# Optimization experiments

Hardware: AMD Instinct MI355X
Metric: run time of the kernel (lower is better)

Reference implementation:

```python
import jax, jax.numpy as jnp
import numpy as np

B, T, ENC, DEC, OUT = 512, 128, 256, 256, 1
Tm1 = T - 1


def setup_inputs() -> dict:
    key = jax.random.key(0)
    ks = jax.random.split(key, 14)
    s = lambda k, shape, scale=0.05: (jax.random.normal(k, shape, dtype=jnp.float32) * scale)
    return {
        "input_encoded": jax.random.normal(ks[0], (B, Tm1, ENC), dtype=jnp.float32),
        "y_history": jax.random.normal(ks[1], (B, Tm1, OUT), dtype=jnp.float32),
        # attn_layer: Linear(2*DEC+ENC -> ENC), Tanh, Linear(ENC -> 1)
        "W_attn1": s(ks[2], (ENC, 2 * DEC + ENC)),
        "b_attn1": s(ks[3], (ENC,)),
        "W_attn2": s(ks[4], (1, ENC)),
        "b_attn2": s(ks[5], (1,)),
        # single-layer LSTM cell (input_size=OUT, hidden=DEC); gate order i,f,g,o
        "W_ih": s(ks[6], (4 * DEC, OUT)),
        "W_hh": s(ks[7], (4 * DEC, DEC)),
        "b_ih": s(ks[8], (4 * DEC,)),
        "b_hh": s(ks[9], (4 * DEC,)),
        # fc: Linear(ENC+OUT -> OUT); torch code re-inits weight ~ N(0,1)
        "W_fc": jax.random.normal(ks[10], (OUT, ENC + OUT), dtype=jnp.float32),
        "b_fc": s(ks[11], (OUT,)),
        # fc_final: Linear(DEC+ENC -> OUT)
        "W_fcf": s(ks[12], (OUT, DEC + ENC)),
        "b_fcf": s(ks[13], (OUT,)),
    }


def reference(input_encoded, y_history, W_attn1, b_attn1, W_attn2, b_attn2,
              W_ih, W_hh, b_ih, b_hh, W_fc, b_fc, W_fcf, b_fcf):
    Bsz, tm1, enc = input_encoded.shape
    dec = W_hh.shape[1]
    h0 = jnp.zeros((Bsz, dec), dtype=input_encoded.dtype)
    c0 = jnp.zeros_like(h0)
    ctx0 = jnp.zeros((Bsz, enc), dtype=input_encoded.dtype)

    def step(carry, y_t):
        h, c, _ = carry  # h, c: [B, DEC]; y_t: [B, OUT]
        hs = jnp.broadcast_to(h[:, None, :], (Bsz, tm1, dec))
        cs = jnp.broadcast_to(c[:, None, :], (Bsz, tm1, dec))
        x = jnp.concatenate([hs, cs, input_encoded], axis=-1)  # [B, Tm1, 2*DEC+ENC]
        score = jnp.tanh(x @ W_attn1.T + b_attn1) @ W_attn2.T + b_attn2  # [B, Tm1, 1]
        attn = jax.nn.softmax(score[..., 0], axis=1)  # [B, Tm1]
        context = jnp.einsum('bt,bte->be', attn, input_encoded)  # [B, ENC]
        y_tilde = jnp.concatenate([context, y_t], axis=1) @ W_fc.T + b_fc  # [B, OUT]
        gates = y_tilde @ W_ih.T + b_ih + h @ W_hh.T + b_hh  # [B, 4*DEC]
        i, f, g, o = jnp.split(gates, 4, axis=1)
        c_new = jax.nn.sigmoid(f) * c + jax.nn.sigmoid(i) * jnp.tanh(g)
        h_new = jax.nn.sigmoid(o) * jnp.tanh(c_new)
        return (h_new, c_new, context), attn

    (h, c, context), attn_rows = jax.lax.scan(
        step, (h0, c0, ctx0), jnp.swapaxes(y_history, 0, 1))
    weight = jnp.swapaxes(attn_rows, 0, 1)  # [B, Tm1, Tm1]
    out = jnp.concatenate([h, context], axis=1) @ W_fcf.T + b_fcf  # [B, OUT]
    return out, weight
```

## Files before the change

kernel.cpp:

```cpp
#include <hip/hip_runtime.h>

typedef _Float16 f16;
typedef _Float16 h2 __attribute__((ext_vector_type(2)));
typedef _Float16 h4 __attribute__((ext_vector_type(4)));
typedef _Float16 h8 __attribute__((ext_vector_type(8)));

#define T127 127

#define H2S(v, i) __builtin_shufflevector(v, v, 2 * (i), 2 * (i) + 1)

__device__ __forceinline__ float rcp_f(float x) { return __builtin_amdgcn_rcpf(x); }

__device__ __forceinline__ float fdot2(h2 a, h2 b, float c) {
  return __builtin_amdgcn_fdot2(a, b, c, false);
}
__device__ __forceinline__ h2 mk2(f16 a, f16 b) { h2 v; v[0] = a; v[1] = b; return v; }

__device__ __forceinline__ float fast_sig(float x) {
  x = fminf(fmaxf(x, -30.f), 30.f);
  return rcp_f(1.f + __expf(-x));
}
__device__ __forceinline__ float fast_tanh(float x) {
  x = fminf(fmaxf(x, -12.f), 12.f);
  float e = __expf(2.f * x);
  return (e - 1.f) * rcp_f(e + 1.f);
}

__device__ __forceinline__ void bar_lds() {
  asm volatile("s_waitcnt lgkmcnt(0)" ::: "memory");
  __builtin_amdgcn_s_barrier();
  asm volatile("" ::: "memory");
}

__global__ void pack_wsU(const float* __restrict__ Wa1, f16* __restrict__ wsU) {
  int tid = blockIdx.x * 256 + threadIdx.x;
  int it = tid >> 9, L = tid & 511;
  int kL = L >> 1, g2 = L & 1;
  const float* src = Wa1 + (size_t)kL * 768 + (it >> 4) * 256 + g2 * 128 + (it & 15) * 8;
  f16* dst = wsU + (size_t)tid * 8;
#pragma unroll
  for (int j = 0; j < 8; ++j) dst[j] = (f16)src[j];
}

__global__ void pack_wsH(const float* __restrict__ Whh, f16* __restrict__ wsH) {
  int tid = blockIdx.x * 256 + threadIdx.x;
  int i = tid >> 10, kk = (tid >> 2) & 255, g = tid & 3;
  const float* src = Whh + (size_t)(g * 256 + kk) * 256 + i * 8;
  f16* dst = wsH + (size_t)tid * 8;
#pragma unroll
  for (int j = 0; j < 8; ++j) dst[j] = (f16)src[j];
}

__global__ __attribute__((amdgpu_flat_work_group_size(512, 512)))
void decoder_kernel(
    const float* __restrict__ enc,
    const float* __restrict__ yhist,
    const float* __restrict__ Wa1,
    const float* __restrict__ ba1,
    const float* __restrict__ Wa2,
    const float* __restrict__ ba2,
    const float* __restrict__ Wih,
    const float* __restrict__ bih,
    const float* __restrict__ bhh,
    const float* __restrict__ Wfc,
    const float* __restrict__ bfc,
    const float* __restrict__ Wfcf,
    const float* __restrict__ bfcf,
    const f16* __restrict__ wsU,
    const f16* __restrict__ wsH,
    float* __restrict__ outp)
{
  __shared__ __align__(16) f16 tE1[2 * 34592];
  __shared__ __align__(16) f16 hch[2][4][136];
  __shared__ __align__(16) float s_arr[2][4][68];
  __shared__ __align__(16) float score_s[2][128];
  __shared__ __align__(16) float p_s[2][128];
  __shared__ __align__(16) float q_s[2][128];
  __shared__ __align__(16) f16 est[8][288];
  __shared__ __align__(16) float w2_lds[256];
  __shared__ __align__(16) float yh_s[2][128];
  __shared__ float ctxq_s[2], red2[16];

  const int L = threadIdx.x;
  const int b0 = blockIdx.x * 2;
  const int kL = L >> 1;
  const int g2 = L & 1;
  const int kk2 = L >> 1;
  const int bbE = L & 1;
  const int g_u = L & 3;

  for (int i = L; i < 1088; i += 512) ((f16*)hch)[i] = (f16)0.f;
  if (L < 256) {
    w2_lds[L] = Wa2[L];
    int bb = L >> 7, tt = L & 127;
    if (tt < T127) yh_s[bb][tt] = yhist[(size_t)(b0 + bb) * T127 + tt];
  }
  float c_reg = 0.f;

  {
    h2 we1[64];
    {
      const float4* wrow = (const float4*)(Wa1 + (size_t)kL * 768 + 512 + g2 * 128);
#pragma unroll
      for (int i = 0; i < 32; ++i) {
        float4 w = wrow[i];
        we1[2 * i]     = mk2((f16)w.x, (f16)w.y);
        we1[2 * i + 1] = mk2((f16)w.z, (f16)w.w);
      }
    }
    const int prow = L >> 6;
    const int lm = L & 63;
    const int sg = lm >> 4;
    const int si = (lm * 4) & 63;

#pragma unroll 1
    for (int tt = 0; tt < 32; ++tt) {
      __syncthreads();
      {
        int bbs = prow >> 2, j4 = prow & 3, j = tt * 4 + j4;
        float4 v = make_float4(0.f, 0.f, 0.f, 0.f);
        if (j < T127)
          v = *(const float4*)(enc + (((size_t)(b0 + bbs)) * T127 + j) * 256 + lm * 4);
        h4 hv; hv[0] = (f16)v.x; hv[1] = (f16)v.y; hv[2] = (f16)v.z; hv[3] = (f16)v.w;
        *(h4*)(&est[prow][0] + sg * 72 + si) = hv;
      }
      __syncthreads();
#pragma unroll 1
      for (int P = 0; P < 8; ++P) {
        int bbs = P >> 2, j4 = P & 3, j = tt * 4 + j4;
        const h8* ep = (const h8*)(&est[P][0] + (2 * g2) * 72);
        const h8* ep2 = (const h8*)(&est[P][0] + (2 * g2 + 1) * 72);
        float a0 = 0.f, a1 = 0.f;
#pragma unroll
        for (int r = 0; r < 8; ++r) {
          h8 e8 = ep[r];
          a0 = fdot2(we1[4 * r + 0], H2S(e8, 0), a0);
          a1 = fdot2(we1[4 * r + 1], H2S(e8, 1), a1);
          a0 = fdot2(we1[4 * r + 2], H2S(e8, 2), a0);
          a1 = fdot2(we1[4 * r + 3], H2S(e8, 3), a1);
        }
#pragma unroll
        for (int r = 0; r < 8; ++r) {
          h8 e8 = ep2[r];
          a0 = fdot2(we1[32 + 4 * r + 0], H2S(e8, 0), a0);
          a1 = fdot2(we1[32 + 4 * r + 1], H2S(e8, 1), a1);
          a0 = fdot2(we1[32 + 4 * r + 2], H2S(e8, 2), a0);
          a1 = fdot2(we1[32 + 4 * r + 3], H2S(e8, 3), a1);
        }
        float acc = a0 + a1;
        acc += __shfl_xor(acc, 1, 64);
        if (g2 == 0 && j < T127) {
          float z = fminf(fmaxf(2.f * acc, -9.f), 9.f);
          tE1[bbs * 34592 + j * 272 + (kL >> 6) * 68 + (kL & 63)] = (f16)__expf(z);
        }
      }
      {
        int bbs = prow >> 2, j4 = prow & 3, j = tt * 4 + j4;
        float4 wp4 = *(const float4*)(Wfc + lm * 4);
        float4 wq4 = *(const float4*)(Wfcf + 256 + lm * 4);
        h4 ev = *(const h4*)(&est[prow][0] + sg * 72 + si);
        float pacc = (float)ev[0] * wp4.x + (float)ev[1] * wp4.y + (float)ev[2] * wp4.z + (float)ev[3] * wp4.w;
        float qacc = (float)ev[0] * wq4.x + (float)ev[1] * wq4.y + (float)ev[2] * wq4.z + (float)ev[3] * wq4.w;
#pragma unroll
        for (int s = 32; s; s >>= 1) {
          pacc += __shfl_xor(pacc, s, 64);
          qacc += __shfl_xor(qacc, s, 64);
        }
        if (lm == 0 && j < T127) { p_s[bbs][j] = pacc; q_s[bbs][j] = qacc; }
      }
    }
  }
  __syncthreads();

  const float b1k = ba1[kL];
  const float wih0 = Wih[kk2];
  const float wih1 = Wih[256 + kk2];
  const float wih2 = Wih[512 + kk2];
  const float wih3 = Wih[768 + kk2];
  const float bia0 = bih[kk2] + bhh[kk2];
  const float bia1 = bih[256 + kk2] + bhh[256 + kk2];
  const float bia2 = bih[512 + kk2] + bhh[512 + kk2];
  const float bia3 = bih[768 + kk2] + bhh[768 + kk2];
  const float ba2v = ba2[0];
  const float wfcy = Wfc[256];
  const float bfc0 = bfc[0];
  const float wfcf_k = Wfcf[kk2];

  const h8* wp = (const h8*)wsU + L;
  const h8* wb = (const h8*)wsH + ((size_t)g2 * 16 * 256 + kk2) * 4;
  const f16* hxb = (const f16*)hch + g2 * 136;

  const int prA = L >> 2;
  const int bbA = prA & 1, jA = prA >> 1;
  const int prB = prA + 128;
  const int prC = prB < 254 ? prB : 253;
  const int bbB2 = prC & 1, jB2 = prC >> 1;
  const h4* tpA = (const h4*)(tE1 + bbA * 34592 + jA * 272 + g_u * 68);
  const h4* tpB = (const h4*)(tE1 + bbB2 * 34592 + jB2 * 272 + g_u * 68);
  const float4* spA = (const float4*)&s_arr[bbA][g_u][0];
  const float4* spB = (const float4*)&s_arr[bbB2][g_u][0];
  const float4* w2p = (const float4*)&w2_lds[g_u * 64];

  float W2q = 0.f;
#pragma unroll
  for (int i = 0; i < 16; ++i) {
    float4 v = w2p[i];
    W2q += v.x + v.y + v.z + v.w;
  }

#pragma unroll 1
  for (int t = 0; t < T127; ++t) {
    float u0a = 0.f, u0b = 0.f, u1a = 0.f, u1b = 0.f;
    {
      h8 a0 = wp[0], a1 = wp[512], a2 = wp[1024], a3 = wp[1536];
#pragma unroll 4
      for (int it = 0; it < 32; ++it) {
        h8 nxt = wp[((it + 4) & 31) * 512];
        const f16* hp = hxb + (it >> 4) * 272 + (it & 15) * 8;
        h8 x = *(const h8*)hp;
        h8 y = *(const h8*)(hp + 544);
        u0a = fdot2(H2S(a0, 0), H2S(x, 0), u0a);
        u0b = fdot2(H2S(a0, 1), H2S(x, 1), u0b);
        u0a = fdot2(H2S(a0, 2), H2S(x, 2), u0a);
        u0b = fdot2(H2S(a0, 3), H2S(x, 3), u0b);
        u1a = fdot2(H2S(a0, 0), H2S(y, 0), u1a);
        u1b = fdot2(H2S(a0, 1), H2S(y, 1), u1b);
        u1a = fdot2(H2S(a0, 2), H2S(y, 2), u1a);
        u1b = fdot2(H2S(a0, 3), H2S(y, 3), u1b);
        a0 = a1; a1 = a2; a2 = a3; a3 = nxt;
      }
    }
    {
      float u0 = u0a + u0b, u1 = u1a + u1b;
      u0 += __shfl_xor(u0, 1, 64);
      u1 += __shfl_xor(u1, 1, 64);
      if (g2 == 0) {
        float z = fminf(fmaxf(2.f * (u0 + b1k), -18.f), 18.f);
        s_arr[0][kL >> 6][kL & 63] = __expf(z);
      } else {
        float z = fminf(fmaxf(2.f * (u1 + b1k), -18.f), 18.f);
        s_arr[1][kL >> 6][kL & 63] = __expf(z);
      }
    }
    h8 A0 = wb[0], A1r = wb[1], A2 = wb[2], A3 = wb[3];
    h8 B0 = wb[1024], B1 = wb[1025], B2 = wb[1026], B3 = wb[1027];
    bar_lds();

    float ghA0 = 0.f, ghA1 = 0.f, ghA2 = 0.f, ghA3 = 0.f;
    float ghB0 = 0.f, ghB1 = 0.f, ghB2 = 0.f, ghB3 = 0.f;
    float accA0 = 0.f, accA1 = 0.f, accB0 = 0.f, accB1 = 0.f;

#define GH8(acc, w, v)                            \
    acc = fdot2(H2S(w, 0), H2S(v, 0), acc);       \
    acc = fdot2(H2S(w, 1), H2S(v, 1), acc);       \
    acc = fdot2(H2S(w, 2), H2S(v, 2), acc);       \
    acc = fdot2(H2S(w, 3), H2S(v, 3), acc);

#define FBODY(C0, C1, C2, C3, II)                                              \
    {                                                                          \
      int ipn = ((II) + 2) & 15;                                               \
      h8 T0 = wb[ipn * 1024 + 0], T1 = wb[ipn * 1024 + 1];                     \
      h8 T2 = wb[ipn * 1024 + 2], T3 = wb[ipn * 1024 + 3];                     \
      h8 x = *(const h8*)(hxb + (II) * 8);                        \
      h8 y = *(const h8*)(hxb + 544 + (II) * 8);                  \
      GH8(ghA0, C0, x)  GH8(ghB0, C0, y)                                       \
      GH8(ghA1, C1, x)  GH8(ghB1, C1, y)                                       \
      GH8(ghA2, C2, x)  GH8(ghB2, C2, y)                                       \
      GH8(ghA3, C3, x)  GH8(ghB3, C3, y)                                       \
      {                                                                        \
        float4 wv = w2p[(II)];                                                 \
        h4 tv = tpA[(II)];                                                     \
        float4 sv = spA[(II)];                                                 \
        accA0 = fmaf(wv.x, rcp_f(fmaf(sv.x, (float)tv[0], 1.f)), accA0);       \
        accA1 = fmaf(wv.y, rcp_f(fmaf(sv.y, (float)tv[1], 1.f)), accA1);       \
        accA0 = fmaf(wv.z, rcp_f(fmaf(sv.z, (float)tv[2], 1.f)), accA0);       \
        accA1 = fmaf(wv.w, rcp_f(fmaf(sv.w, (float)tv[3], 1.f)), accA1);       \
        h4 tw = tpB[(II)];                                                     \
        float4 sw = spB[(II)];                                                 \
        accB0 = fmaf(wv.x, rcp_f(fmaf(sw.x, (float)tw[0], 1.f)), accB0);       \
        accB1 = fmaf(wv.y, rcp_f(fmaf(sw.y, (float)tw[1], 1.f)), accB1);       \
        accB0 = fmaf(wv.z, rcp_f(fmaf(sw.z, (float)tw[2], 1.f)), accB0);       \
        accB1 = fmaf(wv.w, rcp_f(fmaf(sw.w, (float)tw[3], 1.f)), accB1);       \
      }                                                                        \
      C0 = T0; C1 = T1; C2 = T2; C3 = T3;                                      \
    }

#pragma unroll 1
    for (int ih = 0; ih < 8; ++ih) {
      FBODY(A0, A1r, A2, A3, 2 * ih)
      FBODY(B0, B1, B2, B3, 2 * ih + 1)
    }
#undef FBODY
#undef GH8
    {
      float accA = fmaf(-2.f, accA0 + accA1, W2q);
      accA += __shfl_xor(accA, 1, 64);
      accA += __shfl_xor(accA, 2, 64);
      if (g_u == 0) score_s[bbA][jA] = accA + ba2v;
      float accB = fmaf(-2.f, accB0 + accB1, W2q);
      accB += __shfl_xor(accB, 1, 64);
      accB += __shfl_xor(accB, 2, 64);
      if (g_u == 0 && prB < 254) score_s[bbB2][jB2] = accB + ba2v;
    }
    float gh0, gh1, gh2, gh3;
    {
      float s0 = g2 ? ghA0 : ghB0, k0 = g2 ? ghB0 : ghA0;
      float s1 = g2 ? ghA1 : ghB1, k1 = g2 ? ghB1 : ghA1;
      float s2 = g2 ? ghA2 : ghB2, k2v = g2 ? ghB2 : ghA2;
      float s3 = g2 ? ghA3 : ghB3, k3 = g2 ? ghB3 : ghA3;
      gh0 = k0 + __shfl_xor(s0, 1, 64);
      gh1 = k1 + __shfl_xor(s1, 1, 64);
      gh2 = k2v + __shfl_xor(s2, 1, 64);
      gh3 = k3 + __shfl_xor(s3, 1, 64);
    }
    bar_lds();

    float ytil0, ytil1;
    float ra, rb;
    {
      const int ln = L & 63;
      const int wv = L >> 6;
      float e0a = __expf(score_s[0][ln]);
      float e1a = (ln < 63) ? __expf(score_s[0][64 + ln]) : 0.f;
      float e0b = __expf(score_s[1][ln]);
      float e1b = (ln < 63) ? __expf(score_s[1][64 + ln]) : 0.f;
      float sa = e0a + e1a, sb = e0b + e1b;
      float cwa = e0a * p_s[0][ln] + ((ln < 63) ? e1a * p_s[0][64 + ln] : 0.f);
      float cwb = e0b * p_s[1][ln] + ((ln < 63) ? e1b * p_s[1][64 + ln] : 0.f);
#pragma unroll
      for (int s = 32; s; s >>= 1) {
        sa += __shfl_xor(sa, s, 64);
        sb += __shfl_xor(sb, s, 64);
        cwa += __shfl_xor(cwa, s, 64);
        cwb += __shfl_xor(cwb, s, 64);
      }
      ra = rcp_f(sa); rb = rcp_f(sb);
      if (wv == 0) {
        float* wout = outp + 512 + ((size_t)b0 * T127 + t) * T127;
        wout[ln] = e0a * ra;
        if (ln < 63) wout[64 + ln] = e1a * ra;
      } else if (wv == 1) {
        float* wout = outp + 512 + ((size_t)(b0 + 1) * T127 + t) * T127;
        wout[ln] = e0b * rb;
        if (ln < 63) wout[64 + ln] = e1b * rb;
      }
      ytil0 = cwa * ra + wfcy * yh_s[0][t] + bfc0;
      ytil1 = cwb * rb + wfcy * yh_s[1][t] + bfc0;
      if (t == T127 - 1) {
        float cqa = e0a * q_s[0][ln] + ((ln < 63) ? e1a * q_s[0][64 + ln] : 0.f);
        float cqb = e0b * q_s[1][ln] + ((ln < 63) ? e1b * q_s[1][64 + ln] : 0.f);
#pragma unroll
        for (int s = 32; s; s >>= 1) {
          cqa += __shfl_xor(cqa, s, 64);
          cqb += __shfl_xor(cqb, s, 64);
        }
        if (L == 0) { ctxq_s[0] = cqa * ra; ctxq_s[1] = cqb * rb; }
      }
    }

    {
      float yt = bbE ? ytil1 : ytil0;
      float g_i = gh0 + wih0 * yt + bia0;
      float g_f = gh1 + wih1 * yt + bia1;
      float g_g = gh2 + wih2 * yt + bia2;
      float g_o = gh3 + wih3 * yt + bia3;
      float ai = fast_sig(g_i);
      float af = fast_sig(g_f);
      float ag = fast_tanh(g_g);
      float ao = fast_sig(g_o);
      float cn = af * c_reg + ai * ag;
      float hn = ao * fast_tanh(cn);
      c_reg = cn;
      hch[bbE][kk2 >> 7][kk2 & 127] = (f16)hn;
      hch[bbE][2 + (kk2 >> 7)][kk2 & 127] = (f16)cn;
      if (t == T127 - 1) {
        float po = wfcf_k * hn;
        po += __shfl_xor(po, 32, 64);
        po += __shfl_xor(po, 16, 64);
        po += __shfl_xor(po, 8, 64);
        po += __shfl_xor(po, 4, 64);
        po += __shfl_xor(po, 2, 64);
        if ((L & 63) < 2) red2[(L >> 6) * 2 + (L & 1)] = po;
      }
    }
    bar_lds();
  }

  if (L < 2) {
    float o = ctxq_s[L] + bfcf[0];
#pragma unroll
    for (int w = 0; w < 8; ++w) o += red2[w * 2 + L];
    outp[b0 + L] = o;
  }
}

extern "C" void kernel_launch(void* const* d_in, const int* in_sizes, int n_in,
                              void* d_out, int out_size, void* d_ws, size_t ws_size,
                              hipStream_t stream) {
  (void)in_sizes; (void)n_in; (void)out_size; (void)ws_size;
  f16* wsU = (f16*)d_ws;
  f16* wsH = wsU + 131072;
  pack_wsU<<<64, 256, 0, stream>>>((const float*)d_in[2], wsU);
  pack_wsH<<<128, 256, 0, stream>>>((const float*)d_in[7], wsH);
  decoder_kernel<<<256, 512, 0, stream>>>(
      (const float*)d_in[0], (const float*)d_in[1], (const float*)d_in[2],
      (const float*)d_in[3], (const float*)d_in[4], (const float*)d_in[5],
      (const float*)d_in[6], (const float*)d_in[8], (const float*)d_in[9],
      (const float*)d_in[10], (const float*)d_in[11], (const float*)d_in[12],
      (const float*)d_in[13], wsU, wsH, (float*)d_out);
}
```

Before: 1.624 ms.

## Fuse attention-hidden projection with LSTM recurrent matvec before first barrier

Merges the per-step attention projection loop (the h/c part of W_attn1) with the W_hh gate dot products into one pass over the shared h/c vectors, so each h8 load of hxb feeds both. The score-accumulation loop (tanh via rcp) moves into its own loop after the barrier. Weight registers are prefetched before the time loop and rotated across steps, which removes per-step reload latency. This adds register pressure from holding more live weights and accumulators, and it lengthens the work done before the first barrier.

```diff
diff --git a/kernel.cpp b/kernel.cpp
--- a/kernel.cpp
+++ b/kernel.cpp
@@ -208,30 +208,68 @@
     W2q += v.x + v.y + v.z + v.w;
   }
 
+  h8 Uh0 = wp[0], Uh1 = wp[512];
+  h8 Uc0 = wp[16 * 512], Uc1 = wp[17 * 512];
+  h8 A0 = wb[0], A1r = wb[1], A2 = wb[2], A3 = wb[3];
+  h8 B0 = wb[1024], B1 = wb[1025], B2 = wb[1026], B3 = wb[1027];
+
 #pragma unroll 1
   for (int t = 0; t < T127; ++t) {
-    float u0a = 0.f, u0b = 0.f, u1a = 0.f, u1b = 0.f;
-    {
-      h8 a0 = wp[0], a1 = wp[512], a2 = wp[1024], a3 = wp[1536];
-#pragma unroll 4
-      for (int it = 0; it < 32; ++it) {
-        h8 nxt = wp[((it + 4) & 31) * 512];
-        const f16* hp = hxb + (it >> 4) * 272 + (it & 15) * 8;
-        h8 x = *(const h8*)hp;
-        h8 y = *(const h8*)(hp + 544);
-        u0a = fdot2(H2S(a0, 0), H2S(x, 0), u0a);
-        u0b = fdot2(H2S(a0, 1), H2S(x, 1), u0b);
-        u0a = fdot2(H2S(a0, 2), H2S(x, 2), u0a);
-        u0b = fdot2(H2S(a0, 3), H2S(x, 3), u0b);
-        u1a = fdot2(H2S(a0, 0), H2S(y, 0), u1a);
-        u1b = fdot2(H2S(a0, 1), H2S(y, 1), u1b);
-        u1a = fdot2(H2S(a0, 2), H2S(y, 2), u1a);
-        u1b = fdot2(H2S(a0, 3), H2S(y, 3), u1b);
-        a0 = a1; a1 = a2; a2 = a3; a3 = nxt;
-      }
-    }
-    {
-      float u0 = u0a + u0b, u1 = u1a + u1b;
+    float u0 = 0.f, u1 = 0.f;
+    float ghA0 = 0.f, ghA1 = 0.f, ghA2 = 0.f, ghA3 = 0.f;
+    float ghB0 = 0.f, ghB1 = 0.f, ghB2 = 0.f, ghB3 = 0.f;
+
+#define GH8(acc, w, v)                            \
+    acc = fdot2(H2S(w, 0), H2S(v, 0), acc);       \
+    acc = fdot2(H2S(w, 1), H2S(v, 1), acc);       \
+    acc = fdot2(H2S(w, 2), H2S(v, 2), acc);       \
+    acc = fdot2(H2S(w, 3), H2S(v, 3), acc);
+
+#define MBODY(UH, UC, C0, C1, C2, C3, II)                                      \
+    {                                                                          \
+      const int ipn = ((II) + 2) & 15;                                         \
+      const f16* hpb = hxb + (II) * 8;                                         \
+      h8 x = *(const h8*)(hpb);                            \
+      h8 y = *(const h8*)(hpb + 544);                      \
+      GH8(u0, UH, x)                                                           \
+      GH8(u1, UH, y)                                                           \
+      UH = wp[ipn * 512];                                                      \
+      GH8(ghA0, C0, x)  GH8(ghB0, C0, y)                                       \
+      GH8(ghA1, C1, x)  GH8(ghB1, C1, y)                                       \
+      GH8(ghA2, C2, x)  GH8(ghB2, C2, y)                                       \
+      GH8(ghA3, C3, x)  GH8(ghB3, C3, y)                                       \
+      {                                                                        \
+        h8 xc = *(const h8*)(hpb + 272);                   \
+        h8 yc = *(const h8*)(hpb + 816);                   \
+        GH8(u0, UC, xc)                                                        \
+        GH8(u1, UC, yc)                                                        \
+      }                                                                        \
+      UC = wp[(ipn + 16) * 512];                                               \
+      C0 = wb[ipn * 1024 + 0];                                                 \
+      C1 = wb[ipn * 1024 + 1];                                                 \
+      C2 = wb[ipn * 1024 + 2];                                                 \
+      C3 = wb[ipn * 1024 + 3];                                                 \
+    }
+
+#pragma unroll 1
+    for (int ih = 0; ih < 8; ++ih) {
+      MBODY(Uh0, Uc0, A0, A1r, A2, A3, 2 * ih)
+      MBODY(Uh1, Uc1, B0, B1, B2, B3, 2 * ih + 1)
+    }
+#undef MBODY
+
+    float gh0, gh1, gh2, gh3;
+    {
+      float s0 = g2 ? ghA0 : ghB0, k0 = g2 ? ghB0 : ghA0;
+      float s1 = g2 ? ghA1 : ghB1, k1 = g2 ? ghB1 : ghA1;
+      float s2 = g2 ? ghA2 : ghB2, k2v = g2 ? ghB2 : ghA2;
+      float s3 = g2 ? ghA3 : ghB3, k3 = g2 ? ghB3 : ghA3;
+      gh0 = k0 + __shfl_xor(s0, 1, 64);
+      gh1 = k1 + __shfl_xor(s1, 1, 64);
+      gh2 = k2v + __shfl_xor(s2, 1, 64);
+      gh3 = k3 + __shfl_xor(s3, 1, 64);
+    }
+    {
       u0 += __shfl_xor(u0, 1, 64);
       u1 += __shfl_xor(u1, 1, 64);
       if (g2 == 0) {
@@ -242,56 +280,25 @@
         s_arr[1][kL >> 6][kL & 63] = __expf(z);
       }
     }
-    h8 A0 = wb[0], A1r = wb[1], A2 = wb[2], A3 = wb[3];
-    h8 B0 = wb[1024], B1 = wb[1025], B2 = wb[1026], B3 = wb[1027];
     bar_lds();
 
-    float ghA0 = 0.f, ghA1 = 0.f, ghA2 = 0.f, ghA3 = 0.f;
-    float ghB0 = 0.f, ghB1 = 0.f, ghB2 = 0.f, ghB3 = 0.f;
     float accA0 = 0.f, accA1 = 0.f, accB0 = 0.f, accB1 = 0.f;
-
-#define GH8(acc, w, v)                            \
-    acc = fdot2(H2S(w, 0), H2S(v, 0), acc);       \
-    acc = fdot2(H2S(w, 1), H2S(v, 1), acc);       \
-    acc = fdot2(H2S(w, 2), H2S(v, 2), acc);       \
-    acc = fdot2(H2S(w, 3), H2S(v, 3), acc);
-
-#define FBODY(C0, C1, C2, C3, II)                                              \
-    {                                                                          \
-      int ipn = ((II) + 2) & 15;                                               \
-      h8 T0 = wb[ipn * 1024 + 0], T1 = wb[ipn * 1024 + 1];                     \
-      h8 T2 = wb[ipn * 1024 + 2], T3 = wb[ipn * 1024 + 3];                     \
-      h8 x = *(const h8*)(hxb + (II) * 8);                        \
-      h8 y = *(const h8*)(hxb + 544 + (II) * 8);                  \
-      GH8(ghA0, C0, x)  GH8(ghB0, C0, y)                                       \
-      GH8(ghA1, C1, x)  GH8(ghB1, C1, y)                                       \
-      GH8(ghA2, C2, x)  GH8(ghB2, C2, y)                                       \
-      GH8(ghA3, C3, x)  GH8(ghB3, C3, y)                                       \
-      {                                                                        \
-        float4 wv = w2p[(II)];                                                 \
-        h4 tv = tpA[(II)];                                                     \
-        float4 sv = spA[(II)];                                                 \
-        accA0 = fmaf(wv.x, rcp_f(fmaf(sv.x, (float)tv[0], 1.f)), accA0);       \
-        accA1 = fmaf(wv.y, rcp_f(fmaf(sv.y, (float)tv[1], 1.f)), accA1);       \
-        accA0 = fmaf(wv.z, rcp_f(fmaf(sv.z, (float)tv[2], 1.f)), accA0);       \
-        accA1 = fmaf(wv.w, rcp_f(fmaf(sv.w, (float)tv[3], 1.f)), accA1);       \
-        h4 tw = tpB[(II)];                                                     \
-        float4 sw = spB[(II)];                                                 \
-        accB0 = fmaf(wv.x, rcp_f(fmaf(sw.x, (float)tw[0], 1.f)), accB0);       \
-        accB1 = fmaf(wv.y, rcp_f(fmaf(sw.y, (float)tw[1], 1.f)), accB1);       \
-        accB0 = fmaf(wv.z, rcp_f(fmaf(sw.z, (float)tw[2], 1.f)), accB0);       \
-        accB1 = fmaf(wv.w, rcp_f(fmaf(sw.w, (float)tw[3], 1.f)), accB1);       \
-      }                                                                        \
-      C0 = T0; C1 = T1; C2 = T2; C3 = T3;                                      \
-    }
-
-#pragma unroll 1
-    for (int ih = 0; ih < 8; ++ih) {
-      FBODY(A0, A1r, A2, A3, 2 * ih)
-      FBODY(B0, B1, B2, B3, 2 * ih + 1)
-    }
-#undef FBODY
-#undef GH8
+#pragma unroll 4
+    for (int ii = 0; ii < 16; ++ii) {
+      float4 wv = w2p[ii];
+      h4 tv = tpA[ii];
+      float4 sv = spA[ii];
+      accA0 = fmaf(wv.x, rcp_f(fmaf(sv.x, (float)tv[0], 1.f)), accA0);
+      accA1 = fmaf(wv.y, rcp_f(fmaf(sv.y, (float)tv[1], 1.f)), accA1);
+      accA0 = fmaf(wv.z, rcp_f(fmaf(sv.z, (float)tv[2], 1.f)), accA0);
+      accA1 = fmaf(wv.w, rcp_f(fmaf(sv.w, (float)tv[3], 1.f)), accA1);
+      h4 tw = tpB[ii];
+      float4 sw = spB[ii];
+      accB0 = fmaf(wv.x, rcp_f(fmaf(sw.x, (float)tw[0], 1.f)), accB0);
+      accB1 = fmaf(wv.y, rcp_f(fmaf(sw.y, (float)tw[1], 1.f)), accB1);
+      accB0 = fmaf(wv.z, rcp_f(fmaf(sw.z, (float)tw[2], 1.f)), accB0);
+      accB1 = fmaf(wv.w, rcp_f(fmaf(sw.w, (float)tw[3], 1.f)), accB1);
+    }
     {
       float accA = fmaf(-2.f, accA0 + accA1, W2q);
       accA += __shfl_xor(accA, 1, 64);
@@ -301,17 +308,6 @@
       accB += __shfl_xor(accB, 1, 64);
       accB += __shfl_xor(accB, 2, 64);
       if (g_u == 0 && prB < 254) score_s[bbB2][jB2] = accB + ba2v;
-    }
-    float gh0, gh1, gh2, gh3;
-    {
-      float s0 = g2 ? ghA0 : ghB0, k0 = g2 ? ghB0 : ghA0;
-      float s1 = g2 ? ghA1 : ghB1, k1 = g2 ? ghB1 : ghA1;
-      float s2 = g2 ? ghA2 : ghB2, k2v = g2 ? ghB2 : ghA2;
-      float s3 = g2 ? ghA3 : ghB3, k3 = g2 ? ghB3 : ghA3;
-      gh0 = k0 + __shfl_xor(s0, 1, 64);
-      gh1 = k1 + __shfl_xor(s1, 1, 64);
-      gh2 = k2v + __shfl_xor(s2, 1, 64);
-      gh3 = k3 + __shfl_xor(s3, 1, 64);
     }
     bar_lds();
 
```

After: 1.932 ms. +19.0%, slower.
